# Kernel optimization log

Hardware: AMD Instinct MI355X
Metric: run time of the kernel (lower is better)

Reference implementation:

```python
import jax, jax.numpy as jnp
import numpy as np

D = 2048      # hidden dim
H = 16        # heads
BSZ = 4       # batch
L = 2048      # seq len
BASE_DT = 0.1


def setup_inputs() -> dict:
    key = jax.random.key(0)
    ks = jax.random.split(key, 9)
    s = 1.0 / np.sqrt(D)
    x = jax.random.normal(ks[0], (BSZ, L, D), dtype=jnp.float32)
    v = jax.random.normal(ks[1], (BSZ, L, D), dtype=jnp.float32)
    force = jax.random.normal(ks[2], (BSZ, L, D), dtype=jnp.float32)
    WA = jax.random.normal(ks[3], (D, D), dtype=jnp.float32) * s
    bA = jnp.zeros((D,), dtype=jnp.float32)
    WB = jax.random.normal(ks[4], (D, D), dtype=jnp.float32) * s
    bB = jnp.zeros((D,), dtype=jnp.float32)
    Wdt = jax.random.normal(ks[5], (D, D), dtype=jnp.float32) * s
    bdt = jnp.zeros((D,), dtype=jnp.float32)
    # base_dt_scales buffer: 1.5**head_index, repeated head_dim times
    scales = jnp.repeat(1.5 ** jnp.arange(H, dtype=jnp.float32), D // H)
    return {"x": x, "v": v, "force": force, "WA": WA, "bA": bA,
            "WB": WB, "bB": bB, "Wdt": Wdt, "bdt": bdt, "scales": scales}


def _combine(e1, e2):
    # associative op for v_t = a_t * v_{t-1} + b_t ; e1 is the earlier element
    a1, b1 = e1
    a2, b2 = e2
    return a1 * a2, a2 * b1 + b2


def reference(x, v, force, WA, bA, WB, bB, Wdt, bdt, scales):
    # x is LayerNorm-ed in the original but the result is unused; v is unused.
    A = jax.nn.sigmoid(force @ WA + bA)                      # [B, L, D] in (0,1)
    dt = jax.nn.softplus(force @ Wdt + bdt) * BASE_DT * scales  # per-head dt scaling
    B_val = (force @ WB + bB) * dt
    # parallel associative scan over the sequence axis: v_t = A_t v_{t-1} + B_t
    _, v_seq = jax.lax.associative_scan(_combine, (A, B_val), axis=1)
    # second scan has A=1 -> plain prefix sum
    x_seq = jnp.cumsum(v_seq * dt, axis=1)
    return x_seq, v_seq
```

## Files before the change

### kernel.cpp

```cpp
#include <hip/hip_runtime.h>
#include <hip/hip_bf16.h>
#include <cstdint>
#include <cstddef>

#define D_DIM 2048
#define L_SEQ 2048
#define B_SZ 4
#define M_ROWS (B_SZ * L_SEQ)
#define NT_COLS (3 * D_DIM)
#define NCH 16
#define CHUNK (L_SEQ / NCH)

typedef __bf16 bf16_t;
typedef bf16_t bf16x8 __attribute__((ext_vector_type(8)));
typedef float f32x4 __attribute__((ext_vector_type(4)));

__device__ __forceinline__ void gl_lds16(const void* g, void* l) {
    __builtin_amdgcn_global_load_lds(
        (const __attribute__((address_space(1))) unsigned int*)g,
        (__attribute__((address_space(3))) unsigned int*)l, 16, 0, 0);
}

__global__ __launch_bounds__(256) void cvt_bf16_kernel(
    const float* __restrict__ in, bf16_t* __restrict__ out, int n8)
{
    int i = blockIdx.x * 256 + threadIdx.x;
    if (i >= n8) return;
    float4 f0 = ((const float4*)in)[2 * i];
    float4 f1 = ((const float4*)in)[2 * i + 1];
    bf16x8 o;
    o[0] = (bf16_t)f0.x; o[1] = (bf16_t)f0.y; o[2] = (bf16_t)f0.z; o[3] = (bf16_t)f0.w;
    o[4] = (bf16_t)f1.x; o[5] = (bf16_t)f1.y; o[6] = (bf16_t)f1.z; o[7] = (bf16_t)f1.w;
    ((bf16x8*)out)[i] = o;
}

__global__ __launch_bounds__(256) void transpose_w_kernel(
    const float* __restrict__ W0, const float* __restrict__ W1,
    const float* __restrict__ W2, bf16_t* __restrict__ Wt)
{
    __shared__ float tile[32][33];
    const float* W = (blockIdx.z == 0) ? W0 : (blockIdx.z == 1) ? W1 : W2;
    bf16_t* dst = Wt + (size_t)blockIdx.z * D_DIM * D_DIM;
    int j0 = blockIdx.x * 32, k0 = blockIdx.y * 32;
    int tx = threadIdx.x, ty = threadIdx.y;
#pragma unroll
    for (int i = 0; i < 4; i++) {
        int k = k0 + ty + i * 8;
        tile[ty + i * 8][tx] = W[(size_t)k * D_DIM + j0 + tx];
    }
    __syncthreads();
#pragma unroll
    for (int i = 0; i < 4; i++) {
        int j = j0 + ty + i * 8;
        dst[(size_t)j * D_DIM + k0 + tx] = (bf16_t)tile[tx][ty + i * 8];
    }
}

__global__ __launch_bounds__(256) void gemm_fused_kernel(
    const bf16_t* __restrict__ Abf,
    const bf16_t* __restrict__ Wt,
    const float* __restrict__ bA, const float* __restrict__ bdt,
    const float* __restrict__ bB, const float* __restrict__ scales,
    float* __restrict__ outA,
    float* __restrict__ outDT,
    float* __restrict__ outB)
{
    __shared__ bf16_t lds_a[128 * 64];
    __shared__ bf16_t lds_b[128 * 64];

    const int bm0 = blockIdx.x * 128;
    const int bn0 = blockIdx.y * 128;
    const int t = threadIdx.x;
    const int lane = t & 63, w = t >> 6;
    const int wr = (w >> 1) * 64;
    const int wc = (w & 1) * 64;

    f32x4 acc[4][4] = {};

    const int srow = t >> 3;
    const int scol = (((t & 7) ^ ((t >> 3) & 7)) << 3);
    const int frow = lane & 15;
    const int q = lane >> 4;
    const int fx7 = frow & 7;
    const int lof0 = frow * 64 + (((q) ^ fx7) << 3);
    const int lof1 = frow * 64 + (((4 + q) ^ fx7) << 3);

    for (int k0 = 0; k0 < D_DIM; k0 += 64) {
#pragma unroll
        for (int j = 0; j < 4; j++) {
            gl_lds16(Abf + (size_t)(bm0 + j * 32 + srow) * D_DIM + k0 + scol,
                     lds_a + j * 2048 + w * 512);
            gl_lds16(Wt  + (size_t)(bn0 + j * 32 + srow) * D_DIM + k0 + scol,
                     lds_b + j * 2048 + w * 512);
        }
        __syncthreads();

        bf16x8 af[4], bfr[4];
#pragma unroll
        for (int m = 0; m < 4; m++)
            af[m] = *(const bf16x8*)&lds_a[(wr + m * 16) * 64 + lof0];
#pragma unroll
        for (int n = 0; n < 4; n++)
            bfr[n] = *(const bf16x8*)&lds_b[(wc + n * 16) * 64 + lof0];
#pragma unroll
        for (int m = 0; m < 4; m++)
#pragma unroll
            for (int n = 0; n < 4; n++)
                acc[m][n] = __builtin_amdgcn_mfma_f32_16x16x32_bf16(
                    af[m], bfr[n], acc[m][n], 0, 0, 0);
#pragma unroll
        for (int m = 0; m < 4; m++)
            af[m] = *(const bf16x8*)&lds_a[(wr + m * 16) * 64 + lof1];
#pragma unroll
        for (int n = 0; n < 4; n++)
            bfr[n] = *(const bf16x8*)&lds_b[(wc + n * 16) * 64 + lof1];
#pragma unroll
        for (int m = 0; m < 4; m++)
#pragma unroll
            for (int n = 0; n < 4; n++)
                acc[m][n] = __builtin_amdgcn_mfma_f32_16x16x32_bf16(
                    af[m], bfr[n], acc[m][n], 0, 0, 0);
        __syncthreads();
    }

    const int seg = bn0 >> 11;
    const int dbase = (bn0 & 2047) + wc + (lane & 15);
    const int rowbase = bm0 + wr + ((lane >> 4) << 2);

    if (seg == 0) {
        float bias[4];
#pragma unroll
        for (int n = 0; n < 4; n++) bias[n] = bA[dbase + n * 16];
#pragma unroll
        for (int m = 0; m < 4; m++)
#pragma unroll
            for (int n = 0; n < 4; n++)
#pragma unroll
                for (int r = 0; r < 4; r++) {
                    size_t idx = (size_t)(rowbase + m * 16 + r) * D_DIM + dbase + n * 16;
                    outA[idx] = 1.0f / (1.0f + __expf(-(acc[m][n][r] + bias[n])));
                }
    } else if (seg == 1) {
        float bias[4], sc[4];
#pragma unroll
        for (int n = 0; n < 4; n++) { bias[n] = bdt[dbase + n * 16]; sc[n] = scales[dbase + n * 16]; }
#pragma unroll
        for (int m = 0; m < 4; m++)
#pragma unroll
            for (int n = 0; n < 4; n++)
#pragma unroll
                for (int r = 0; r < 4; r++) {
                    size_t idx = (size_t)(rowbase + m * 16 + r) * D_DIM + dbase + n * 16;
                    float xx = acc[m][n][r] + bias[n];
                    float sp = xx > 0.f ? xx + log1pf(__expf(-xx)) : log1pf(__expf(xx));
                    outDT[idx] = sp * 0.1f * sc[n];
                }
    } else {
        float bias[4];
#pragma unroll
        for (int n = 0; n < 4; n++) bias[n] = bB[dbase + n * 16];
#pragma unroll
        for (int m = 0; m < 4; m++)
#pragma unroll
            for (int n = 0; n < 4; n++)
#pragma unroll
                for (int r = 0; r < 4; r++) {
                    size_t idx = (size_t)(rowbase + m * 16 + r) * D_DIM + dbase + n * 16;
                    outB[idx] = acc[m][n][r] + bias[n];
                }
    }
}

__global__ __launch_bounds__(256) void scan_pass1_kernel(
    const float* __restrict__ Aarr, const float* __restrict__ Braw,
    const float* __restrict__ dtv, float4* __restrict__ agg)
{
    int pp = blockIdx.x * 256 + threadIdx.x;
    int dp = (pp & 1023) << 1;
    int c = (pp >> 10) & (NCH - 1);
    int b = pp >> 14;
    size_t base = ((size_t)(b * L_SEQ + c * CHUNK)) * D_DIM + dp;
    float P0 = 1.f, R0 = 0.f, U0 = 0.f, W0 = 0.f;
    float P1 = 1.f, R1 = 0.f, U1 = 0.f, W1 = 0.f;
#pragma unroll 4
    for (int tt = 0; tt < CHUNK; tt++) {
        size_t idx = base + (size_t)tt * D_DIM;
        float2 a2  = *(const float2*)&Aarr[idx];
        float2 rb2 = *(const float2*)&Braw[idx];
        float2 dt2 = *(const float2*)&dtv[idx];
        float bv0 = rb2.x * dt2.x, bv1 = rb2.y * dt2.y;
        float da0 = dt2.x * a2.x,  da1 = dt2.y * a2.y;
        R0 = da0 * P0 + R0;  W0 = da0 * U0 + dt2.x * bv0 + W0;
        U0 = a2.x * U0 + bv0;  P0 = a2.x * P0;
        R1 = da1 * P1 + R1;  W1 = da1 * U1 + dt2.y * bv1 + W1;
        U1 = a2.y * U1 + bv1;  P1 = a2.y * P1;
    }
    int ch = ((b * NCH + c) << 11) + dp;
    agg[ch]     = make_float4(P0, R0, U0, W0);
    agg[ch + 1] = make_float4(P1, R1, U1, W1);
}

__global__ __launch_bounds__(256) void scan_pass2_kernel(
    const float4* __restrict__ agg, float2* __restrict__ pre)
{
    int tid = blockIdx.x * 256 + threadIdx.x;
    int d = tid & (D_DIM - 1);
    int b = tid >> 11;
    float v = 0.f, x = 0.f;
#pragma unroll
    for (int c = 0; c < NCH; c++) {
        int i = ((b * NCH + c) << 11) + d;
        float4 g = agg[i];
        pre[i] = make_float2(v, x);
        float vn = g.x * v + g.z;
        x = g.y * v + x + g.w;
        v = vn;
    }
}

__global__ __launch_bounds__(256) void scan_pass3_kernel(
    const float* __restrict__ dtv, const float2* __restrict__ pre,
    float* __restrict__ xout, float* __restrict__ vout)
{
    int pp = blockIdx.x * 256 + threadIdx.x;
    int dp = (pp & 1023) << 1;
    int c = (pp >> 10) & (NCH - 1);
    int b = pp >> 14;
    int ch = ((b * NCH + c) << 11) + dp;
    float4 pv = *(const float4*)&pre[ch];
    float v0 = pv.x, x0 = pv.y, v1 = pv.z, x1 = pv.w;
    size_t base = ((size_t)(b * L_SEQ + c * CHUNK)) * D_DIM + dp;
#pragma unroll 4
    for (int tt = 0; tt < CHUNK; tt++) {
        size_t idx = base + (size_t)tt * D_DIM;
        float2 a2  = *(const float2*)&xout[idx];
        float2 rb2 = *(const float2*)&vout[idx];
        float2 dt2 = *(const float2*)&dtv[idx];
        v0 = a2.x * v0 + rb2.x * dt2.x;
        x0 = x0 + v0 * dt2.x;
        v1 = a2.y * v1 + rb2.y * dt2.y;
        x1 = x1 + v1 * dt2.y;
        *(float2*)&vout[idx] = make_float2(v0, v1);
        *(float2*)&xout[idx] = make_float2(x0, x1);
    }
}

extern "C" void kernel_launch(void* const* d_in, const int* in_sizes, int n_in,
                              void* d_out, int out_size, void* d_ws, size_t ws_size,
                              hipStream_t stream) {
    const float* force  = (const float*)d_in[2];
    const float* WA     = (const float*)d_in[3];
    const float* bA     = (const float*)d_in[4];
    const float* WB     = (const float*)d_in[5];
    const float* bB     = (const float*)d_in[6];
    const float* Wdt    = (const float*)d_in[7];
    const float* bdt    = (const float*)d_in[8];
    const float* scales = (const float*)d_in[9];

    float* xout = (float*)d_out;
    float* vout = xout + (size_t)M_ROWS * D_DIM;

    char* ws = (char*)d_ws;
    bf16_t* fbf = (bf16_t*)ws;
    bf16_t* wt  = (bf16_t*)(ws + (size_t)33554432);
    float*  dtv = (float*)(ws + (size_t)33554432 + 25165824);
    float4* agg = (float4*)(ws + (size_t)33554432 + 25165824 + 67108864);
    float2* pre = (float2*)(ws + (size_t)33554432 + 25165824 + 67108864 + 2097152);

    {
        int n8 = M_ROWS * D_DIM / 8;
        cvt_bf16_kernel<<<n8 / 256, 256, 0, stream>>>(force, fbf, n8);
    }
    {
        dim3 grid(D_DIM / 32, D_DIM / 32, 3), block(32, 8);
        transpose_w_kernel<<<grid, block, 0, stream>>>(WA, Wdt, WB, wt);
    }
    {
        dim3 grid(M_ROWS / 128, NT_COLS / 128);
        gemm_fused_kernel<<<grid, 256, 0, stream>>>(fbf, wt, bA, bdt, bB, scales,
                                                    xout, dtv, vout);
    }
    scan_pass1_kernel<<<(B_SZ * NCH * D_DIM / 2) / 256, 256, 0, stream>>>(xout, vout, dtv, agg);
    scan_pass2_kernel<<<(B_SZ * D_DIM) / 256, 256, 0, stream>>>(agg, pre);
    scan_pass3_kernel<<<(B_SZ * NCH * D_DIM / 2) / 256, 256, 0, stream>>>(dtv, pre, xout, vout);
}
```

Before: 457.3 us.

## Double-buffer LDS tiles in the fused GEMM and raise MFMA wave priority

The GEMM main loop now uses two LDS buffers for the A and W tiles. The next K-tile's global-to-LDS loads are issued before computing on the current tile, with one barrier per tile instead of two. The MFMA blocks are wrapped in s_setprio so matrix work gets scheduling priority. The aim is to hide global load latency behind compute. In exchange, LDS use per block doubles to 64 KB, which can lower occupancy.

```diff
diff --git a/kernel.cpp b/kernel.cpp
--- a/kernel.cpp
+++ b/kernel.cpp
@@ -20,6 +20,9 @@
         (const __attribute__((address_space(1))) unsigned int*)g,
         (__attribute__((address_space(3))) unsigned int*)l, 16, 0, 0);
 }
+
+#define BAR()    asm volatile("s_barrier" ::: "memory")
+#define VMCNT0() asm volatile("s_waitcnt vmcnt(0)" ::: "memory")
 
 __global__ __launch_bounds__(256) void cvt_bf16_kernel(
     const float* __restrict__ in, bf16_t* __restrict__ out, int n8)
@@ -56,6 +59,39 @@
     }
 }
 
+#define STAGE(LA, LB, T) {                                                     \
+    const size_t kofs_ = (size_t)(T) * 64;                                     \
+    _Pragma("unroll") for (int j = 0; j < 4; j++) {                            \
+        gl_lds16(Abf + (size_t)(bm0 + j * 32 + srow) * D_DIM + kofs_ + scol,   \
+                 (LA) + j * 2048 + w * 512);                                   \
+        gl_lds16(Wt  + (size_t)(bn0 + j * 32 + srow) * D_DIM + kofs_ + scol,   \
+                 (LB) + j * 2048 + w * 512);                                   \
+    } }
+
+#define COMPUTE(LA, LB) {                                                      \
+    bf16x8 af[4], bfr[4];                                                      \
+    _Pragma("unroll") for (int m = 0; m < 4; m++)                              \
+        af[m] = *(const bf16x8*)&(LA)[(wr + m * 16) * 64 + lof0];              \
+    _Pragma("unroll") for (int n = 0; n < 4; n++)                              \
+        bfr[n] = *(const bf16x8*)&(LB)[(wc + n * 16) * 64 + lof0];             \
+    __builtin_amdgcn_s_setprio(1);                                             \
+    _Pragma("unroll") for (int m = 0; m < 4; m++)                              \
+        _Pragma("unroll") for (int n = 0; n < 4; n++)                          \
+            acc[m][n] = __builtin_amdgcn_mfma_f32_16x16x32_bf16(               \
+                af[m], bfr[n], acc[m][n], 0, 0, 0);                            \
+    __builtin_amdgcn_s_setprio(0);                                             \
+    _Pragma("unroll") for (int m = 0; m < 4; m++)                              \
+        af[m] = *(const bf16x8*)&(LA)[(wr + m * 16) * 64 + lof1];              \
+    _Pragma("unroll") for (int n = 0; n < 4; n++)                              \
+        bfr[n] = *(const bf16x8*)&(LB)[(wc + n * 16) * 64 + lof1];             \
+    __builtin_amdgcn_s_setprio(1);                                             \
+    _Pragma("unroll") for (int m = 0; m < 4; m++)                              \
+        _Pragma("unroll") for (int n = 0; n < 4; n++)                          \
+            acc[m][n] = __builtin_amdgcn_mfma_f32_16x16x32_bf16(               \
+                af[m], bfr[n], acc[m][n], 0, 0, 0);                            \
+    __builtin_amdgcn_s_setprio(0);                                             \
+}
+
 __global__ __launch_bounds__(256) void gemm_fused_kernel(
     const bf16_t* __restrict__ Abf,
     const bf16_t* __restrict__ Wt,
@@ -65,8 +101,8 @@
     float* __restrict__ outDT,
     float* __restrict__ outB)
 {
-    __shared__ bf16_t lds_a[128 * 64];
-    __shared__ bf16_t lds_b[128 * 64];
+    __shared__ bf16_t lds_a[2][128 * 64];
+    __shared__ bf16_t lds_b[2][128 * 64];
 
     const int bm0 = blockIdx.x * 128;
     const int bn0 = blockIdx.y * 128;
@@ -85,42 +121,21 @@
     const int lof0 = frow * 64 + (((q) ^ fx7) << 3);
     const int lof1 = frow * 64 + (((4 + q) ^ fx7) << 3);
 
-    for (int k0 = 0; k0 < D_DIM; k0 += 64) {
-#pragma unroll
-        for (int j = 0; j < 4; j++) {
-            gl_lds16(Abf + (size_t)(bm0 + j * 32 + srow) * D_DIM + k0 + scol,
-                     lds_a + j * 2048 + w * 512);
-            gl_lds16(Wt  + (size_t)(bn0 + j * 32 + srow) * D_DIM + k0 + scol,
-                     lds_b + j * 2048 + w * 512);
-        }
-        __syncthreads();
-
-        bf16x8 af[4], bfr[4];
-#pragma unroll
-        for (int m = 0; m < 4; m++)
-            af[m] = *(const bf16x8*)&lds_a[(wr + m * 16) * 64 + lof0];
-#pragma unroll
-        for (int n = 0; n < 4; n++)
-            bfr[n] = *(const bf16x8*)&lds_b[(wc + n * 16) * 64 + lof0];
-#pragma unroll
-        for (int m = 0; m < 4; m++)
-#pragma unroll
-            for (int n = 0; n < 4; n++)
-                acc[m][n] = __builtin_amdgcn_mfma_f32_16x16x32_bf16(
-                    af[m], bfr[n], acc[m][n], 0, 0, 0);
-#pragma unroll
-        for (int m = 0; m < 4; m++)
-            af[m] = *(const bf16x8*)&lds_a[(wr + m * 16) * 64 + lof1];
-#pragma unroll
-        for (int n = 0; n < 4; n++)
-            bfr[n] = *(const bf16x8*)&lds_b[(wc + n * 16) * 64 + lof1];
-#pragma unroll
-        for (int m = 0; m < 4; m++)
-#pragma unroll
-            for (int n = 0; n < 4; n++)
-                acc[m][n] = __builtin_amdgcn_mfma_f32_16x16x32_bf16(
-                    af[m], bfr[n], acc[m][n], 0, 0, 0);
-        __syncthreads();
+    STAGE(lds_a[0], lds_b[0], 0);
+    VMCNT0();
+    BAR();
+
+#pragma unroll 1
+    for (int i = 0; i < 16; ++i) {
+        const int tt = 2 * i;
+        STAGE(lds_a[1], lds_b[1], tt + 1);
+        COMPUTE(lds_a[0], lds_b[0]);
+        VMCNT0();
+        BAR();
+        if (i < 15) STAGE(lds_a[0], lds_b[0], tt + 2);
+        COMPUTE(lds_a[1], lds_b[1]);
+        VMCNT0();
+        BAR();
     }
 
     const int seg = bn0 >> 11;
```

Measured after the change: 426.4 us. 6.8% less time.
